# Performance work log

Measured on AMD Instinct MI355X. Metric: run time of the kernel, lower is better.

## Reference

```python
import jax, jax.numpy as jnp
import numpy as np

DISP_W, MAT_W, CD_W = 1.0, 0.1, 0.5
CHUNK = 512


def _min_dists(a, b):
    # a: [B, Na, 3], b: [B, Nb, 3] -> per-point min squared distance [B, Na]
    B, Na, _ = a.shape
    a_chunks = jnp.swapaxes(a.reshape(B, Na // CHUNK, CHUNK, 3), 0, 1)  # [nc, B, chunk, 3]

    def body(carry, ac):  # ac: [B, chunk, 3]
        d = jnp.sum((ac[:, :, None, :] - b[:, None, :, :]) ** 2, axis=-1)  # [B, chunk, Nb]
        return carry, jnp.min(d, axis=-1)

    _, mins = jax.lax.scan(body, 0, a_chunks)  # [nc, B, chunk]
    return jnp.moveaxis(mins, 0, 1).reshape(B, Na)


def chamfer_distance(pred, target):
    min_p2t = _min_dists(pred, target)
    min_t2p = _min_dists(target, pred)
    return (min_p2t.mean(axis=1) + min_t2p.mean(axis=1)).mean()


def setup_inputs() -> dict:
    key = jax.random.key(0)
    k1, k2, k3, k4, k5 = jax.random.split(key, 5)
    B, N = 4, 8192
    return {
        "pred_disp": jax.random.normal(k1, (B, N, 3), dtype=jnp.float32),
        "pred_mat": jax.random.normal(k2, (B, 2), dtype=jnp.float32),
        "target_disp": jax.random.normal(k3, (B, N, 3), dtype=jnp.float32),
        "target_mat": jax.random.normal(k4, (B, 2), dtype=jnp.float32),
        "template": jax.random.normal(k5, (B, N, 3), dtype=jnp.float32),
    }


def reference(pred_disp, pred_mat, target_disp, target_mat, template):
    disp_loss = jnp.mean(jnp.abs(pred_disp - target_disp))
    mat_loss = jnp.mean((pred_mat - target_mat) ** 2)
    pred_pos = template + pred_disp
    target_pos = template + target_disp
    cd = chamfer_distance(pred_pos, target_pos)
    total = DISP_W * disp_loss + MAT_W * mat_loss + CD_W * cd
    return total
```

## Files before the change

### kernel.cpp

```cpp
#include <hip/hip_runtime.h>

#define DISP_W 1.0f
#define MAT_W  0.1f
#define CD_W   0.5f

typedef _Float16 half8 __attribute__((ext_vector_type(8)));
typedef float f32x16 __attribute__((ext_vector_type(16)));
typedef float f32x4  __attribute__((ext_vector_type(4)));

constexpr int BB = 4;
constexpr int NN = 8192;
constexpr int THREADS = 256;
constexpr int IB = 128;
constexpr int JR = 1024;
constexpr int NIB = NN / IB;
constexpr int NJB = NN / JR;
constexpr int NCHUNK = JR / 32;
constexpr int NPTS = 2 * BB * NN;
constexpr int GRID = 2 * BB * NIB * NJB;
constexpr int RSTRIDE = 36;


__global__ __launch_bounds__(256)
void build_frags(const float* __restrict__ pred_disp,
                 const float* __restrict__ target_disp,
                 const float* __restrict__ tmpl,
                 half8* __restrict__ fragA,
                 half8* __restrict__ fragBhi,
                 half8* __restrict__ fragBlo,
                 float* __restrict__ out)
{
    int p = blockIdx.x * 256 + threadIdx.x;
    if (p == 0) out[0] = 0.0f;
    int c = p >> 15;
    int b = (p >> 13) & (BB - 1);
    int n = p & (NN - 1);

    const float* dp = (c ? target_disp : pred_disp) + (size_t)b * NN * 3;
    const float* tp = tmpl + (size_t)b * NN * 3;

    int n3 = n * 3;
    float x = tp[n3 + 0] + dp[n3 + 0];
    float y = tp[n3 + 1] + dp[n3 + 1];
    float z = tp[n3 + 2] + dp[n3 + 2];
    float cc = fmaf(x, x, fmaf(y, y, z * z));

    _Float16 xh = (_Float16)x;  _Float16 xl = (_Float16)(x - (float)xh);
    _Float16 yh = (_Float16)y;  _Float16 yl = (_Float16)(y - (float)yh);
    _Float16 zh = (_Float16)z;  _Float16 zl = (_Float16)(z - (float)zh);
    _Float16 ch = (_Float16)cc; _Float16 cl = (_Float16)(cc - (float)ch);

    float ux = -2.0f * x, uy = -2.0f * y, uz = -2.0f * z;
    _Float16 uxh = (_Float16)ux; _Float16 uxl = (_Float16)(ux - (float)uxh);
    _Float16 uyh = (_Float16)uy; _Float16 uyl = (_Float16)(uy - (float)uyh);
    _Float16 uzh = (_Float16)uz; _Float16 uzl = (_Float16)(uz - (float)uzh);

    const _Float16 one  = (_Float16)1.0f;
    const _Float16 zero = (_Float16)0.0f;

    half8 aHi = {xh, yh, zh, xh, yh, zh, xl, yl};
    half8 aLo = {zl, ch, cl, one, one, zero, zero, zero};
    half8 bHi = {uxh, uyh, uzh, uxl, uyl, uzl, uxh, uyh};
    half8 bLo = {uzh, one, one, ch, cl, zero, zero, zero};

    fragA[(size_t)p * 2 + 0] = aHi;
    fragA[(size_t)p * 2 + 1] = aLo;
    fragBhi[p] = bHi;
    fragBlo[p] = bLo;
}

__global__ __launch_bounds__(THREADS, 2)
void chamfer_mfma(const half8* __restrict__ fragA,
                  const half8* __restrict__ fragBhi,
                  const half8* __restrict__ fragBlo,
                  float* __restrict__ rowpart)
{
    __shared__ __align__(16) char lds_raw[32768];
    half8* sBhi = (half8*)lds_raw;
    half8* sBlo = (half8*)(lds_raw + 16384);

    int bx = blockIdx.x;
    int jBlk = bx & (NJB - 1);
    int iBlk = (bx >> 3) & (NIB - 1);
    int b    = (bx >> 9) & (BB - 1);
    int dir  = bx >> 11;
    int cA = dir, cB = dir ^ 1;

    const int tid  = threadIdx.x;
    const int lane = tid & 63;
    const int w    = tid >> 6;
    const int hi   = lane >> 5;
    const int li   = lane & 31;

    size_t pB = ((size_t)cB * BB + b) * NN + (size_t)jBlk * JR;
    const half8* gHi = fragBhi + pB;
    const half8* gLo = fragBlo + pB;
    #pragma unroll
    for (int t = 0; t < JR / THREADS; ++t) {
        int idx = t * THREADS + tid;
        sBhi[idx] = gHi[idx];
        sBlo[idx] = gLo[idx];
    }

    int i0 = iBlk * IB + w * 32 + li;
    half8 aF = fragA[(((size_t)cA * BB + b) * NN + i0) * 2 + hi];

    __syncthreads();

    f32x16 kZero = {0.f,0.f,0.f,0.f, 0.f,0.f,0.f,0.f, 0.f,0.f,0.f,0.f, 0.f,0.f,0.f,0.f};
    const half8* baseB = hi ? sBlo : sBhi;
    float rm0[16], rm1[16];
    #pragma unroll
    for (int r = 0; r < 16; ++r) { rm0[r] = 1.0e30f; rm1[r] = 1.0e30f; }

    #pragma unroll 4
    for (int c = 0; c < NCHUNK; c += 2) {
        half8 b0 = baseB[(c + 0) * 32 + li];
        half8 b1 = baseB[(c + 1) * 32 + li];
        f32x16 a0 = __builtin_amdgcn_mfma_f32_32x32x16_f16(aF, b0, kZero, 0, 0, 0);
        f32x16 a1 = __builtin_amdgcn_mfma_f32_32x32x16_f16(aF, b1, kZero, 0, 0, 0);
        #pragma unroll
        for (int r = 0; r < 16; ++r)
            rm0[r] = fminf(rm0[r], a0[r]);
        #pragma unroll
        for (int r = 0; r < 16; ++r)
            rm1[r] = fminf(rm1[r], a1[r]);
    }
    #pragma unroll
    for (int r = 0; r < 16; ++r) rm0[r] = fminf(rm0[r], rm1[r]);

    __syncthreads();
    float* scr = (float*)lds_raw;
    int wbase = w * (32 * RSTRIDE);
    int cbase = wbase + hi * 4 * RSTRIDE + li;
    #pragma unroll
    for (int r = 0; r < 16; ++r)
        scr[cbase + ((r & 3) + 8 * (r >> 2)) * RSTRIDE] = rm0[r];
    __syncthreads();

    const f32x4* rp = (const f32x4*)&scr[wbase + (lane & 31) * RSTRIDE];
    f32x4 q0 = rp[0], q1 = rp[1], q2 = rp[2], q3 = rp[3];
    f32x4 q4 = rp[4], q5 = rp[5], q6 = rp[6], q7 = rp[7];
    f32x4 m4;
    #pragma unroll
    for (int k = 0; k < 4; ++k)
        m4[k] = fminf(fminf(fminf(q0[k], q1[k]), fminf(q2[k], q3[k])),
                      fminf(fminf(q4[k], q5[k]), fminf(q6[k], q7[k])));
    float m = fminf(fminf(m4[0], m4[1]), fminf(m4[2], m4[3]));

    if (lane < 32) {
        size_t base = ((size_t)(dir * BB + b) * NJB + jBlk) * NN
                    + (size_t)iBlk * IB + w * 32;
        rowpart[base + lane] = m;
    }
}

__global__ __launch_bounds__(256)
void final_reduce(const float* __restrict__ pred_disp,
                  const float* __restrict__ target_disp,
                  const float* __restrict__ pred_mat,
                  const float* __restrict__ target_mat,
                  const float* __restrict__ rowpart,
                  float* __restrict__ out)
{
    const int NDISP = BB * NN * 3;
    const int NROWS = 2 * BB * NN;

    int gtid = blockIdx.x * blockDim.x + threadIdx.x;
    int gstride = gridDim.x * blockDim.x;

    float dsum = 0.0f;
    for (int i = gtid; i < NDISP; i += gstride)
        dsum += fabsf(pred_disp[i] - target_disp[i]);

    float msum = 0.0f;
    for (int t = gtid; t < NROWS; t += gstride) {
        int db = t >> 13;
        int i  = t & (NN - 1);
        const float* p = rowpart + (size_t)db * NJB * NN + i;
        float m = 1.0e30f;
        #pragma unroll
        for (int jb = 0; jb < NJB; ++jb)
            m = fminf(m, p[(size_t)jb * NN]);
        msum += fmaxf(m, 0.0f);
    }

    float acc = dsum * (DISP_W / (float)NDISP)
              + msum * (CD_W / (float)(BB * NN));

    if (gtid < 2 * BB) {
        float d = pred_mat[gtid] - target_mat[gtid];
        acc += d * d * (MAT_W / (float)(2 * BB));
    }

    for (int off = 32; off > 0; off >>= 1)
        acc += __shfl_down(acc, off, 64);

    __shared__ float wsum[4];
    if ((threadIdx.x & 63) == 0) wsum[threadIdx.x >> 6] = acc;
    __syncthreads();
    if (threadIdx.x == 0)
        atomicAdd(out, wsum[0] + wsum[1] + wsum[2] + wsum[3]);
}

extern "C" void kernel_launch(void* const* d_in, const int* in_sizes, int n_in,
                              void* d_out, int out_size, void* d_ws, size_t ws_size,
                              hipStream_t stream) {
    const float* pred_disp   = (const float*)d_in[0];
    const float* pred_mat    = (const float*)d_in[1];
    const float* target_disp = (const float*)d_in[2];
    const float* target_mat  = (const float*)d_in[3];
    const float* tmpl        = (const float*)d_in[4];

    half8* fragA   = (half8*)d_ws;
    half8* fragBhi = fragA + (size_t)NPTS * 2;
    half8* fragBlo = fragBhi + NPTS;
    float* rowpart = (float*)(fragBlo + NPTS);
    float* out = (float*)d_out;

    build_frags<<<NPTS / 256, 256, 0, stream>>>(pred_disp, target_disp, tmpl,
                                                fragA, fragBhi, fragBlo, out);
    chamfer_mfma<<<GRID, THREADS, 0, stream>>>(fragA, fragBhi, fragBlo, rowpart);
    final_reduce<<<256, 256, 0, stream>>>(pred_disp, target_disp, pred_mat, target_mat,
                                          rowpart, out);
}
```

Before: 38.47 us.

## Loop each block over all target tiles to compute full row minima in-kernel

Each block of the chamfer kernel now walks all eight target tiles, staging each into LDS in turn, and keeps a running per-row minimum. This removes the per-tile partial-minimum buffer and the eight-way min in the final reduction. The grid shrinks eightfold, so there is less parallelism and latency hiding, and the tile loads are serialized with barriers rather than overlapped with compute. The inner loop is also unrolled to four MFMAs per step.

```diff
diff --git a/kernel.cpp b/kernel.cpp
--- a/kernel.cpp
+++ b/kernel.cpp
@@ -17,7 +17,7 @@
 constexpr int NJB = NN / JR;
 constexpr int NCHUNK = JR / 32;
 constexpr int NPTS = 2 * BB * NN;
-constexpr int GRID = 2 * BB * NIB * NJB;
+constexpr int GRID = 2 * BB * NIB;
 constexpr int RSTRIDE = 36;
 
 
@@ -73,17 +73,16 @@
 void chamfer_mfma(const half8* __restrict__ fragA,
                   const half8* __restrict__ fragBhi,
                   const half8* __restrict__ fragBlo,
-                  float* __restrict__ rowpart)
+                  float* __restrict__ rowmin)
 {
     __shared__ __align__(16) char lds_raw[32768];
     half8* sBhi = (half8*)lds_raw;
     half8* sBlo = (half8*)(lds_raw + 16384);
 
     int bx = blockIdx.x;
-    int jBlk = bx & (NJB - 1);
-    int iBlk = (bx >> 3) & (NIB - 1);
-    int b    = (bx >> 9) & (BB - 1);
-    int dir  = bx >> 11;
+    int iBlk = bx & (NIB - 1);
+    int b    = (bx >> 6) & (BB - 1);
+    int dir  = bx >> 8;
     int cA = dir, cB = dir ^ 1;
 
     const int tid  = threadIdx.x;
@@ -92,50 +91,56 @@
     const int hi   = lane >> 5;
     const int li   = lane & 31;
 
-    size_t pB = ((size_t)cB * BB + b) * NN + (size_t)jBlk * JR;
+    int i0 = iBlk * IB + w * 32 + li;
+    half8 aF = fragA[(((size_t)cA * BB + b) * NN + i0) * 2 + hi];
+
+    size_t pB = ((size_t)cB * BB + b) * NN;
     const half8* gHi = fragBhi + pB;
     const half8* gLo = fragBlo + pB;
+
+    f32x16 kZero = {0.f,0.f,0.f,0.f, 0.f,0.f,0.f,0.f, 0.f,0.f,0.f,0.f, 0.f,0.f,0.f,0.f};
+    float rm[16];
     #pragma unroll
-    for (int t = 0; t < JR / THREADS; ++t) {
-        int idx = t * THREADS + tid;
-        sBhi[idx] = gHi[idx];
-        sBlo[idx] = gLo[idx];
+    for (int r = 0; r < 16; ++r) rm[r] = 1.0e30f;
+
+    for (int j = 0; j < NJB; ++j) {
+        const half8* srcHi = gHi + (size_t)j * JR;
+        const half8* srcLo = gLo + (size_t)j * JR;
+        #pragma unroll
+        for (int t = 0; t < JR / THREADS; ++t) {
+            int idx = t * THREADS + tid;
+            sBhi[idx] = srcHi[idx];
+            sBlo[idx] = srcLo[idx];
+        }
+        __syncthreads();
+
+        const half8* baseB = hi ? sBlo : sBhi;
+        #pragma unroll 2
+        for (int c = 0; c < NCHUNK; c += 4) {
+            half8 b0 = baseB[(c + 0) * 32 + li];
+            half8 b1 = baseB[(c + 1) * 32 + li];
+            half8 b2 = baseB[(c + 2) * 32 + li];
+            half8 b3 = baseB[(c + 3) * 32 + li];
+            f32x16 a0 = __builtin_amdgcn_mfma_f32_32x32x16_f16(aF, b0, kZero, 0, 0, 0);
+            f32x16 a1 = __builtin_amdgcn_mfma_f32_32x32x16_f16(aF, b1, kZero, 0, 0, 0);
+            f32x16 a2 = __builtin_amdgcn_mfma_f32_32x32x16_f16(aF, b2, kZero, 0, 0, 0);
+            f32x16 a3 = __builtin_amdgcn_mfma_f32_32x32x16_f16(aF, b3, kZero, 0, 0, 0);
+            #pragma unroll
+            for (int r = 0; r < 16; ++r)
+                rm[r] = fminf(rm[r], fminf(a0[r], a1[r]));
+            #pragma unroll
+            for (int r = 0; r < 16; ++r)
+                rm[r] = fminf(rm[r], fminf(a2[r], a3[r]));
+        }
+        __syncthreads();
     }
 
-    int i0 = iBlk * IB + w * 32 + li;
-    half8 aF = fragA[(((size_t)cA * BB + b) * NN + i0) * 2 + hi];
-
-    __syncthreads();
-
-    f32x16 kZero = {0.f,0.f,0.f,0.f, 0.f,0.f,0.f,0.f, 0.f,0.f,0.f,0.f, 0.f,0.f,0.f,0.f};
-    const half8* baseB = hi ? sBlo : sBhi;
-    float rm0[16], rm1[16];
-    #pragma unroll
-    for (int r = 0; r < 16; ++r) { rm0[r] = 1.0e30f; rm1[r] = 1.0e30f; }
-
-    #pragma unroll 4
-    for (int c = 0; c < NCHUNK; c += 2) {
-        half8 b0 = baseB[(c + 0) * 32 + li];
-        half8 b1 = baseB[(c + 1) * 32 + li];
-        f32x16 a0 = __builtin_amdgcn_mfma_f32_32x32x16_f16(aF, b0, kZero, 0, 0, 0);
-        f32x16 a1 = __builtin_amdgcn_mfma_f32_32x32x16_f16(aF, b1, kZero, 0, 0, 0);
-        #pragma unroll
-        for (int r = 0; r < 16; ++r)
-            rm0[r] = fminf(rm0[r], a0[r]);
-        #pragma unroll
-        for (int r = 0; r < 16; ++r)
-            rm1[r] = fminf(rm1[r], a1[r]);
-    }
-    #pragma unroll
-    for (int r = 0; r < 16; ++r) rm0[r] = fminf(rm0[r], rm1[r]);
-
-    __syncthreads();
     float* scr = (float*)lds_raw;
     int wbase = w * (32 * RSTRIDE);
     int cbase = wbase + hi * 4 * RSTRIDE + li;
     #pragma unroll
     for (int r = 0; r < 16; ++r)
-        scr[cbase + ((r & 3) + 8 * (r >> 2)) * RSTRIDE] = rm0[r];
+        scr[cbase + ((r & 3) + 8 * (r >> 2)) * RSTRIDE] = rm[r];
     __syncthreads();
 
     const f32x4* rp = (const f32x4*)&scr[wbase + (lane & 31) * RSTRIDE];
@@ -149,9 +154,8 @@
     float m = fminf(fminf(m4[0], m4[1]), fminf(m4[2], m4[3]));
 
     if (lane < 32) {
-        size_t base = ((size_t)(dir * BB + b) * NJB + jBlk) * NN
-                    + (size_t)iBlk * IB + w * 32;
-        rowpart[base + lane] = m;
+        size_t base = ((size_t)(dir * BB + b)) * NN + (size_t)iBlk * IB + w * 32;
+        rowmin[base + lane] = m;
     }
 }
 
@@ -160,7 +164,7 @@
                   const float* __restrict__ target_disp,
                   const float* __restrict__ pred_mat,
                   const float* __restrict__ target_mat,
-                  const float* __restrict__ rowpart,
+                  const float* __restrict__ rowmin,
                   float* __restrict__ out)
 {
     const int NDISP = BB * NN * 3;
@@ -174,16 +178,8 @@
         dsum += fabsf(pred_disp[i] - target_disp[i]);
 
     float msum = 0.0f;
-    for (int t = gtid; t < NROWS; t += gstride) {
-        int db = t >> 13;
-        int i  = t & (NN - 1);
-        const float* p = rowpart + (size_t)db * NJB * NN + i;
-        float m = 1.0e30f;
-        #pragma unroll
-        for (int jb = 0; jb < NJB; ++jb)
-            m = fminf(m, p[(size_t)jb * NN]);
-        msum += fmaxf(m, 0.0f);
-    }
+    for (int t = gtid; t < NROWS; t += gstride)
+        msum += fmaxf(rowmin[t], 0.0f);
 
     float acc = dsum * (DISP_W / (float)NDISP)
               + msum * (CD_W / (float)(BB * NN));
@@ -215,12 +211,12 @@
     half8* fragA   = (half8*)d_ws;
     half8* fragBhi = fragA + (size_t)NPTS * 2;
     half8* fragBlo = fragBhi + NPTS;
-    float* rowpart = (float*)(fragBlo + NPTS);
+    float* rowmin  = (float*)(fragBlo + NPTS);
     float* out = (float*)d_out;
 
     build_frags<<<NPTS / 256, 256, 0, stream>>>(pred_disp, target_disp, tmpl,
                                                 fragA, fragBhi, fragBlo, out);
-    chamfer_mfma<<<GRID, THREADS, 0, stream>>>(fragA, fragBhi, fragBlo, rowpart);
+    chamfer_mfma<<<GRID, THREADS, 0, stream>>>(fragA, fragBhi, fragBlo, rowmin);
     final_reduce<<<256, 256, 0, stream>>>(pred_disp, target_disp, pred_mat, target_mat,
-                                          rowpart, out);
-}
+                                          rowmin, out);
+}
```

After: 52.22 us. +35.8%, slower.
